# Kernel optimization log

Hardware: AMD Instinct MI355X
Metric: run time of the kernel (lower is better)

The kernel has to match this reference:

```python
import jax, jax.numpy as jnp
import numpy as np

D_MODEL = 512
NHEAD = 8
HEAD_DIM = D_MODEL // NHEAD  # 64
BUCKETS = 32                 # lsh_hash_bucket_size; hashes >= 32 never attended (faithful to source loop)
N_HASHES = 2
B, T = 2, 2048


def setup_inputs() -> dict:
    key = jax.random.key(0)
    ks = jax.random.split(key, 14)
    s = 1.0 / np.sqrt(D_MODEL)
    sh = 1.0 / np.sqrt(HEAD_DIM)
    return {
        "query": jax.random.normal(ks[0], (B, T, D_MODEL), dtype=jnp.float32),
        "key": jax.random.normal(ks[1], (B, T, D_MODEL), dtype=jnp.float32),
        "value": jax.random.normal(ks[2], (B, T, D_MODEL), dtype=jnp.float32),
        "Wq": jax.random.normal(ks[3], (D_MODEL, D_MODEL), dtype=jnp.float32) * s,
        "bq": jnp.zeros((D_MODEL,), jnp.float32),
        "Wk": jax.random.normal(ks[4], (D_MODEL, D_MODEL), dtype=jnp.float32) * s,
        "bk": jnp.zeros((D_MODEL,), jnp.float32),
        "Wv": jax.random.normal(ks[5], (D_MODEL, D_MODEL), dtype=jnp.float32) * s,
        "bv": jnp.zeros((D_MODEL,), jnp.float32),
        "Wo": jax.random.normal(ks[6], (D_MODEL, D_MODEL), dtype=jnp.float32) * s,
        "bo": jnp.zeros((D_MODEL,), jnp.float32),
        "lsh_W": jax.random.normal(ks[7], (N_HASHES, HEAD_DIM, HEAD_DIM), dtype=jnp.float32) * sh,
        "lsh_b": jax.random.normal(ks[8], (N_HASHES, HEAD_DIM), dtype=jnp.float32) * sh,
    }


def reference(query, key, value, Wq, bq, Wk, bk, Wv, bv, Wo, bo, lsh_W, lsh_b):
    B0, Nt, E = query.shape
    H, Dh = NHEAD, E // NHEAD

    def lin(x, W, b):  # torch nn.Linear: x @ W.T + b
        return x @ W.T + b

    # Source transposes (0,1) then reshape(B0, Nt, H, Dh); reshape on the
    # contiguous transposed tensor == jnp reshape of swapaxes result.
    q = lin(jnp.swapaxes(query, 0, 1), Wq, bq).reshape(B0, Nt, H, Dh).transpose(0, 2, 1, 3)
    k = lin(jnp.swapaxes(key, 0, 1), Wk, bk).reshape(B0, Nt, H, Dh).transpose(0, 2, 1, 3)
    v = lin(jnp.swapaxes(value, 0, 1), Wv, bv).reshape(B0, Nt, H, Dh).transpose(0, 2, 1, 3)

    scale = 1.0 / jnp.sqrt(jnp.asarray(Dh, q.dtype))
    neg = jnp.finfo(q.dtype).min
    acc = jnp.zeros_like(q)
    for i in range(N_HASHES):
        # argmax(softmax(x)) == argmax(x)
        qh = jnp.argmax(q @ lsh_W[i].T + lsh_b[i], axis=-1)  # [B,H,T]
        kh = jnp.argmax(k @ lsh_W[i].T + lsh_b[i], axis=-1)  # [B,H,T]
        # attend only within same bucket AND bucket id < BUCKETS (source loops 0..BUCKETS-1)
        mask = (qh[..., :, None] == kh[..., None, :]) & (qh[..., :, None] < BUCKETS)
        scores = jnp.einsum('bhtd,bhsd->bhts', q, k) * scale
        probs = jax.nn.softmax(jnp.where(mask, scores, neg), axis=-1)
        valid = mask.any(axis=-1)  # queries with >=1 key in-bucket; others stay zero
        out_i = jnp.einsum('bhts,bhsd->bhtd', probs, v)
        acc = acc + jnp.where(valid[..., None], out_i, jnp.zeros((), q.dtype))
    out = acc / N_HASHES  # mean over hash rounds

    out = out.transpose(0, 2, 1, 3).reshape(B0, Nt, E)
    out = lin(out, Wo, bo)
    return jnp.swapaxes(out, 0, 1)  # [Nt, B0, E]
```

## Files before the change

kernel.cpp:

```cpp
#include <hip/hip_runtime.h>
#include <stdint.h>
#include <math.h>


#define T_ 2048
#define E_ 512
#define H_ 8
#define DH_ 64
#define B_ 2
#define M_ 4096
#define NROUND 2
#define NBUCKET 32
#define NSEG 32
#define MAXTASK 5120

typedef short v8s __attribute__((ext_vector_type(8)));
typedef _Float16 v8h __attribute__((ext_vector_type(8)));
typedef float v4f __attribute__((ext_vector_type(4)));

__device__ __forceinline__ float bf2f(uint16_t u) {
  union { uint32_t i; float f; } v; v.i = ((uint32_t)u) << 16; return v.f;
}
__device__ __forceinline__ uint16_t f2bf(float f) {
  union { float fv; uint32_t i; } v; v.fv = f;
  uint32_t x = v.i;
  x += 0x7fffu + ((x >> 16) & 1u);
  return (uint16_t)(x >> 16);
}
__device__ __forceinline__ void split8(const float4 a, const float4 b,
                                       v8s& h, v8s& l) {
  const float x[8] = {a.x, a.y, a.z, a.w, b.x, b.y, b.z, b.w};
#pragma unroll
  for (int j = 0; j < 8; j++) {
    const uint16_t hh = f2bf(x[j]);
    h[j] = (short)hh;
    l[j] = (short)f2bf(x[j] - bf2f(hh));
  }
}
__device__ __forceinline__ void split2h8(const float4 a, const float4 b,
                                         v8h& h, v8h& l) {
  const float x[8] = {a.x, a.y, a.z, a.w, b.x, b.y, b.z, b.w};
#pragma unroll
  for (int j = 0; j < 8; j++) {
    const float xv = x[j];
    const _Float16 hh = (fabsf(xv) < 6.1035156e-5f) ? (_Float16)0.0f
                                                    : (_Float16)xv;
    const float r = xv - (float)hh;
    h[j] = hh;
    l[j] = (_Float16)(r * 4096.0f);
  }
}

__global__ __launch_bounds__(256) void prep_kernel(
    const float* __restrict__ Xq, const float* __restrict__ Xk,
    const float* __restrict__ Xv,
    const float* __restrict__ Wq, const float* __restrict__ Wk,
    const float* __restrict__ Wv, const float* __restrict__ Wo,
    const float* __restrict__ lshW,
    uint16_t* __restrict__ Xqh, uint16_t* __restrict__ Xql,
    uint16_t* __restrict__ Xkh, uint16_t* __restrict__ Xkl,
    uint16_t* __restrict__ Xvh, uint16_t* __restrict__ Xvl,
    uint16_t* __restrict__ Wqh, uint16_t* __restrict__ Wql,
    uint16_t* __restrict__ Wkh, uint16_t* __restrict__ Wkl,
    uint16_t* __restrict__ Wvh, uint16_t* __restrict__ Wvl,
    uint16_t* __restrict__ Woh, uint16_t* __restrict__ Wol,
    uint16_t* __restrict__ Lwh, uint16_t* __restrict__ Lwl,
    float* __restrict__ attn, int* __restrict__ cnt)
{
  const int bid = blockIdx.x;
  const int tid = threadIdx.x;

  if (bid < 3072) {
    const int sel = bid >> 10;
    const float* X = (sel == 0) ? Xq : (sel == 1) ? Xk : Xv;
    uint16_t* H = (sel == 0) ? Xqh : (sel == 1) ? Xkh : Xvh;
    uint16_t* L = (sel == 0) ? Xql : (sel == 1) ? Xkl : Xvl;
    const int e = ((bid & 1023) * 256 + tid) * 8;
    const int p = e >> 9, k = e & 511;
    const long src = ((long)(p & 1) * T_ + (p >> 1)) * E_ + k;
    const float4 a = *(const float4*)(X + src);
    const float4 b = *(const float4*)(X + src + 4);
    v8h h, l;
    split2h8(a, b, h, l);
    const long to = ((long)((p >> 5) * 32 + (k >> 5) * 2 + ((p >> 4) & 1)) * 64
                     + ((k >> 3) & 3) * 16 + (p & 15)) * 8;
    *(v8h*)(H + to) = h;
    *(v8h*)(L + to) = l;
    return;
  }

  if (bid < 3584) {
    const int wsel = (bid - 3072) >> 7;
    const int e = (((bid - 3072) & 127) * 256 + tid) * 8;
    const int n = e >> 9, k = e & 511;
    const long to = ((long)((n >> 4) * 16 + (k >> 5)) * 64
                     + ((k >> 3) & 3) * 16 + (n & 15)) * 8;
    if (wsel < 3) {
      const float* S = (wsel == 0) ? Wq : (wsel == 1) ? Wk : Wv;
      const float4 a = *(const float4*)(S + e);
      const float4 b = *(const float4*)(S + e + 4);
      v8h h, l;
      split2h8(a, b, h, l);
      uint16_t* H = (wsel == 0) ? Wqh : (wsel == 1) ? Wkh : Wvh;
      uint16_t* L = (wsel == 0) ? Wql : (wsel == 1) ? Wkl : Wvl;
      *(v8h*)(H + to) = h;
      *(v8h*)(L + to) = l;
    } else {
      const float4 a = *(const float4*)(Wo + e);
      const float4 b = *(const float4*)(Wo + e + 4);
      v8s h, l;
      split8(a, b, h, l);
      *(v8s*)(Woh + to) = h;
      *(v8s*)(Wol + to) = l;
    }
    return;
  }

  if (bid < 4608) {
    float4* a4 = (float4*)attn;
    const int g = (bid - 3584) * 512 + tid * 2;
    a4[g] = make_float4(0.f, 0.f, 0.f, 0.f);
    a4[g + 1] = make_float4(0.f, 0.f, 0.f, 0.f);
    return;
  }

  for (int i = tid; i < 2 * NSEG * NBUCKET + 1; i += 256) cnt[i] = 0;
  for (int i = tid; i < NROUND * DH_ * DH_; i += 256) {
    const float xv = lshW[i];
    const _Float16 hh = (fabsf(xv) < 6.1035156e-5f) ? (_Float16)0.0f
                                                    : (_Float16)xv;
    const float r = xv - (float)hh;
    *(_Float16*)(Lwh + i) = hh;
    *(_Float16*)(Lwl + i) = (_Float16)(r * 4096.0f);
  }
}

__global__ __launch_bounds__(256) void proj_mfma(
    const uint16_t* __restrict__ Aqh, const uint16_t* __restrict__ Aql,
    const uint16_t* __restrict__ Akh, const uint16_t* __restrict__ Akl,
    const uint16_t* __restrict__ Avh, const uint16_t* __restrict__ Avl,
    const uint16_t* __restrict__ Bqh, const uint16_t* __restrict__ Bql,
    const uint16_t* __restrict__ Bkh, const uint16_t* __restrict__ Bkl,
    const uint16_t* __restrict__ Bvh, const uint16_t* __restrict__ Bvl,
    const float* __restrict__ bq, const float* __restrict__ bk,
    const float* __restrict__ bv,
    float* __restrict__ Qo, float* __restrict__ Ko, float* __restrict__ Vo)
{
  const uint16_t *Ah, *Al, *Bh, *Bl;
  const float* bias; float* C;
  if (blockIdx.z == 0)      { Ah = Aqh; Al = Aql; Bh = Bqh; Bl = Bql; bias = bq; C = Qo; }
  else if (blockIdx.z == 1) { Ah = Akh; Al = Akl; Bh = Bkh; Bl = Bkl; bias = bk; C = Ko; }
  else                      { Ah = Avh; Al = Avl; Bh = Bvh; Bl = Bvl; bias = bv; C = Vo; }

  const int wid = threadIdx.x >> 6, lane = threadIdx.x & 63;
  const int mb = blockIdx.x * 4 + wid;
  const int nb0 = blockIdx.y * 4;
  const int m0 = mb * 32, n0 = blockIdx.y * 64;
  const int l15 = lane & 15, quad = lane >> 4;

  const long aB = (long)mb * 16384 + lane * 8;
  long bB[4];
#pragma unroll
  for (int j = 0; j < 4; j++) bB[j] = (long)(nb0 + j) * 8192 + lane * 8;

  v4f accH[2][4] = {};
  v4f accX[2][4] = {};

  v8h ah0 = *(const v8h*)(Ah + aB);
  v8h ah1 = *(const v8h*)(Ah + aB + 512);
  v8h al0 = *(const v8h*)(Al + aB);
  v8h al1 = *(const v8h*)(Al + aB + 512);
  v8h bh[4], bl[4];
#pragma unroll
  for (int j = 0; j < 4; j++) {
    bh[j] = *(const v8h*)(Bh + bB[j]);
    bl[j] = *(const v8h*)(Bl + bB[j]);
  }

  for (int ks = 0; ks < 16; ks++) {
    const int kn = (ks + 1) & 15;
    const v8h nah0 = *(const v8h*)(Ah + aB + kn * 1024);
    const v8h nah1 = *(const v8h*)(Ah + aB + kn * 1024 + 512);
    const v8h nal0 = *(const v8h*)(Al + aB + kn * 1024);
    const v8h nal1 = *(const v8h*)(Al + aB + kn * 1024 + 512);
    v8h nbh[4], nbl[4];
#pragma unroll
    for (int j = 0; j < 4; j++) {
      nbh[j] = *(const v8h*)(Bh + bB[j] + kn * 512);
      nbl[j] = *(const v8h*)(Bl + bB[j] + kn * 512);
    }

#pragma unroll
    for (int j = 0; j < 4; j++) {
      accH[0][j] = __builtin_amdgcn_mfma_f32_16x16x32_f16(ah0, bh[j], accH[0][j], 0, 0, 0);
      accH[1][j] = __builtin_amdgcn_mfma_f32_16x16x32_f16(ah1, bh[j], accH[1][j], 0, 0, 0);
    }
#pragma unroll
    for (int j = 0; j < 4; j++) {
      accX[0][j] = __builtin_amdgcn_mfma_f32_16x16x32_f16(ah0, bl[j], accX[0][j], 0, 0, 0);
      accX[1][j] = __builtin_amdgcn_mfma_f32_16x16x32_f16(ah1, bl[j], accX[1][j], 0, 0, 0);
    }
#pragma unroll
    for (int j = 0; j < 4; j++) {
      accX[0][j] = __builtin_amdgcn_mfma_f32_16x16x32_f16(al0, bh[j], accX[0][j], 0, 0, 0);
      accX[1][j] = __builtin_amdgcn_mfma_f32_16x16x32_f16(al1, bh[j], accX[1][j], 0, 0, 0);
    }

    ah0 = nah0; al0 = nal0; ah1 = nah1; al1 = nal1;
#pragma unroll
    for (int j = 0; j < 4; j++) { bh[j] = nbh[j]; bl[j] = nbl[j]; }
  }

#pragma unroll
  for (int i = 0; i < 2; i++)
#pragma unroll
    for (int j = 0; j < 4; j++) {
      const int colg = n0 + j * 16 + l15;
      const float bb = bias[colg];
#pragma unroll
      for (int r = 0; r < 4; r++) {
        const int mm = m0 + i * 16 + quad * 4 + r;
        C[(long)mm * E_ + colg] =
            accH[i][j][r] + accX[i][j][r] * (1.0f / 4096.0f) + bb;
      }
    }
}

__global__ __launch_bounds__(256) void mfma_gemm(
    const float* __restrict__ A,
    const uint16_t* __restrict__ Bht, const uint16_t* __restrict__ Blt,
    const float* __restrict__ bias, float* __restrict__ C)
{
  const int wid = threadIdx.x >> 6, lane = threadIdx.x & 63;
  const int m0 = (blockIdx.x * 4 + wid) * 32;
  const int nb0 = blockIdx.y * 4;
  const int n0 = blockIdx.y * 64;
  const int l15 = lane & 15, quad = lane >> 4;

  const long sa0 = (long)(m0 + l15) * E_ + quad * 8;
  const long sa1 = sa0 + 16L * E_;
  long bB[4];
#pragma unroll
  for (int j = 0; j < 4; j++) bB[j] = (long)(nb0 + j) * 8192 + lane * 8;

  v4f acc[2][4] = {};
  for (int ks = 0; ks < 16; ks++) {
    const int k0 = ks * 32;
    v8s ah0, al0, ah1, al1;
    split8(*(const float4*)(A + sa0 + k0), *(const float4*)(A + sa0 + k0 + 4),
           ah0, al0);
    split8(*(const float4*)(A + sa1 + k0), *(const float4*)(A + sa1 + k0 + 4),
           ah1, al1);
    v8s bh[4], bl[4];
#pragma unroll
    for (int j = 0; j < 4; j++) {
      bh[j] = *(const v8s*)(Bht + bB[j] + ks * 512);
      bl[j] = *(const v8s*)(Blt + bB[j] + ks * 512);
    }
#pragma unroll
    for (int j = 0; j < 4; j++) {
      acc[0][j] = __builtin_amdgcn_mfma_f32_16x16x32_bf16(ah0, bh[j], acc[0][j], 0, 0, 0);
      acc[1][j] = __builtin_amdgcn_mfma_f32_16x16x32_bf16(ah1, bh[j], acc[1][j], 0, 0, 0);
    }
#pragma unroll
    for (int j = 0; j < 4; j++) {
      acc[0][j] = __builtin_amdgcn_mfma_f32_16x16x32_bf16(ah0, bl[j], acc[0][j], 0, 0, 0);
      acc[1][j] = __builtin_amdgcn_mfma_f32_16x16x32_bf16(ah1, bl[j], acc[1][j], 0, 0, 0);
    }
#pragma unroll
    for (int j = 0; j < 4; j++) {
      acc[0][j] = __builtin_amdgcn_mfma_f32_16x16x32_bf16(al0, bh[j], acc[0][j], 0, 0, 0);
      acc[1][j] = __builtin_amdgcn_mfma_f32_16x16x32_bf16(al1, bh[j], acc[1][j], 0, 0, 0);
    }
  }

#pragma unroll
  for (int i = 0; i < 2; i++)
#pragma unroll
    for (int j = 0; j < 4; j++) {
      const int colg = n0 + j * 16 + l15;
      const float bb = bias[colg];
#pragma unroll
      for (int r = 0; r < 4; r++) {
        const int mm = m0 + i * 16 + quad * 4 + r;
        const int crow = (mm & (T_ - 1)) * B_ + (mm >> 11);
        C[(long)crow * E_ + colg] = acc[i][j][r] + bb;
      }
    }
}

__global__ __launch_bounds__(256) void hash_mfma(
    const float* __restrict__ Q, const float* __restrict__ K,
    const uint16_t* __restrict__ Lwh, const uint16_t* __restrict__ Lwl,
    const float* __restrict__ lshb,
    int* __restrict__ qh, int* __restrict__ kh,
    int* __restrict__ qcnt, int* __restrict__ kcnt)
{
  const int comb = blockIdx.y;
  const int src = comb >> 1, r = comb & 1;
  const float* X = src ? K : Q;
  int* outh = src ? kh : qh;
  int* cnt  = src ? kcnt : qcnt;

  const int wid = threadIdx.x >> 6, lane = threadIdx.x & 63;
  const int m0 = (blockIdx.x * 4 + wid) * 32;
  const int l15 = lane & 15, quad = lane >> 4;

  v8h bh[4][2], bl[4][2];
#pragma unroll
  for (int n = 0; n < 4; n++)
#pragma unroll
    for (int k = 0; k < 2; k++) {
      const int o = r * (DH_ * DH_) + (n * 16 + l15) * DH_ + k * 32 + quad * 8;
      bh[n][k] = *(const v8h*)(Lwh + o);
      bl[n][k] = *(const v8h*)(Lwl + o);
    }

  v4f accH[2][4] = {};
  v4f accX[2][4] = {};
#pragma unroll
  for (int k = 0; k < 2; k++) {
    const long a0 = (long)(m0 + l15) * DH_ + k * 32 + quad * 8;
    const long a1 = a0 + 16L * DH_;
    v8h ah0, al0, ah1, al1;
    split2h8(*(const float4*)(X + a0), *(const float4*)(X + a0 + 4), ah0, al0);
    split2h8(*(const float4*)(X + a1), *(const float4*)(X + a1 + 4), ah1, al1);
#pragma unroll
    for (int n = 0; n < 4; n++) {
      accH[0][n] = __builtin_amdgcn_mfma_f32_16x16x32_f16(ah0, bh[n][k], accH[0][n], 0, 0, 0);
      accH[1][n] = __builtin_amdgcn_mfma_f32_16x16x32_f16(ah1, bh[n][k], accH[1][n], 0, 0, 0);
      accX[0][n] = __builtin_amdgcn_mfma_f32_16x16x32_f16(ah0, bl[n][k], accX[0][n], 0, 0, 0);
      accX[1][n] = __builtin_amdgcn_mfma_f32_16x16x32_f16(ah1, bl[n][k], accX[1][n], 0, 0, 0);
      accX[0][n] = __builtin_amdgcn_mfma_f32_16x16x32_f16(al0, bh[n][k], accX[0][n], 0, 0, 0);
      accX[1][n] = __builtin_amdgcn_mfma_f32_16x16x32_f16(al1, bh[n][k], accX[1][n], 0, 0, 0);
    }
  }

  float bb[4];
#pragma unroll
  for (int n = 0; n < 4; n++) bb[n] = lshb[r * DH_ + n * 16 + l15];

#pragma unroll
  for (int i = 0; i < 2; i++)
#pragma unroll
    for (int reg = 0; reg < 4; reg++) {
      float bv = -INFINITY; int bi = 0x7fffffff;
#pragma unroll
      for (int n = 0; n < 4; n++) {
        const float v = accH[i][n][reg] + accX[i][n][reg] * (1.0f / 4096.0f)
                        + bb[n];
        const int idx = n * 16 + l15;
        if (v > bv || (v == bv && idx < bi)) { bv = v; bi = idx; }
      }
#pragma unroll
      for (int d = 8; d >= 1; d >>= 1) {
        const float ov = __shfl_xor(bv, d);
        const int oi = __shfl_xor(bi, d);
        if (ov > bv || (ov == bv && oi < bi)) { bv = ov; bi = oi; }
      }
      if (l15 == 0) {
        const int hr = m0 + i * 16 + quad * 4 + reg;
        const int p = hr >> 3, hh = hr & 7;
        const int bt = p >> 11, t = p & (T_ - 1);
        const int seg = r * 16 + bt * H_ + hh;
        outh[seg * T_ + t] = bi;
        if (bi < NBUCKET) atomicAdd(&cnt[seg * NBUCKET + bi], 1);
      }
    }
}

__global__ __launch_bounds__(1024) void scan_kernel(
    const int* __restrict__ kcnt, int* __restrict__ koff,
    int* __restrict__ kcur,
    const int* __restrict__ qcnt, int* __restrict__ qoff,
    int* __restrict__ qcur,
    int* __restrict__ ntasks, int* __restrict__ tasks)
{
  const int tid = threadIdx.x;
  const int isq = blockIdx.x;
  const int seg = tid >> 5;
  const int b   = tid & 31;
  const int* cnt = isq ? qcnt : kcnt;
  int* off = isq ? qoff : koff;
  int* cur = isq ? qcur : kcur;

  const int c = cnt[seg * NBUCKET + b];

  int s = c;
#pragma unroll
  for (int d = 1; d < 32; d <<= 1) {
    const int t = __shfl_up(s, d, 32);
    if (b >= d) s += t;
  }
  const int excl = s - c;
  off[seg * (NBUCKET + 1) + b] = excl;
  cur[seg * NBUCKET + b] = excl;
  if (b == 31) off[seg * (NBUCKET + 1) + NBUCKET] = s;

  if (isq) {
    const int nt = (c + 15) >> 4;
    const int lane = tid & 63;
    int ws = nt;
#pragma unroll
    for (int d = 1; d < 64; d <<= 1) {
      const int t = __shfl_up(ws, d, 64);
      if (lane >= d) ws += t;
    }
    const int wtotal = __shfl(ws, 63, 64);
    int base = 0;
    if (lane == 63 && wtotal > 0) base = atomicAdd(ntasks, wtotal);
    base = __shfl(base, 63, 64);
    const int my = base + ws - nt;
    for (int i = 0; i < nt; i++)
      tasks[my + i] = (seg << 16) | (b << 8) | i;
  }
}

__global__ __launch_bounds__(256) void scatter2_kernel(
    const int* __restrict__ kh, const int* __restrict__ qh,
    int* __restrict__ kcur, int* __restrict__ qcur,
    int* __restrict__ klist, int* __restrict__ qlist)
{
  const int idx = blockIdx.x * 256 + threadIdx.x;
  const int y = blockIdx.y;
  const int* hsh = y ? qh : kh;
  int* cur = y ? qcur : kcur;
  int* list = y ? qlist : klist;
  const int v = hsh[idx];
  if (v < NBUCKET) {
    const int seg = idx >> 11;
    const int pos = atomicAdd(&cur[seg * NBUCKET + v], 1);
    list[seg * T_ + pos] = idx & (T_ - 1);
  }
}

__global__ __launch_bounds__(256) void attn_task(
    const float* __restrict__ Q, const float* __restrict__ K,
    const float* __restrict__ V,
    const int* __restrict__ qlist, const int* __restrict__ qoff,
    const int* __restrict__ klist, const int* __restrict__ koff,
    const int* __restrict__ tasks, const int* __restrict__ ntasks,
    float* __restrict__ attn)
{
  __shared__ __align__(16) float QPs[16 * 68];
  __shared__ __align__(16) float Ks[64 * 68];
  __shared__ __align__(16) float Vs[64 * 68];

  if ((int)blockIdx.x >= *ntasks) return;
  const int tk = tasks[blockIdx.x];
  const int seg = tk >> 16, bucket = (tk >> 8) & 255, qt = tk & 255;
  const int ctx = seg & 15;
  const int b = ctx >> 3, h = ctx & 7;

  const int qlo = qoff[seg * (NBUCKET + 1) + bucket] + qt * 16;
  const int nqt = min(16, qoff[seg * (NBUCKET + 1) + bucket + 1] - qlo);
  const int klo = koff[seg * (NBUCKET + 1) + bucket];
  const int nk  = koff[seg * (NBUCKET + 1) + bucket + 1] - klo;
  if (nk == 0) return;

  const int tid = threadIdx.x;
  const int qrow = tid >> 4, col = tid & 15;
  const float* Qb = Q + ((long)b * T_) * E_ + h * DH_;
  const float* Kb = K + ((long)b * T_) * E_ + h * DH_;
  const float* Vb = V + ((long)b * T_) * E_ + h * DH_;
  const int* ql = qlist + seg * T_;
  const int* kl = klist + seg * T_;

  {
    float4 v = make_float4(0.f, 0.f, 0.f, 0.f);
    if (qrow < nqt) v = *(const float4*)(Qb + (long)ql[qlo + qrow] * E_ + col * 4);
    *(float4*)&QPs[qrow * 68 + col * 4] = v;
  }
  __syncthreads();
  float4 qreg[16];
#pragma unroll
  for (int i = 0; i < 16; i++) qreg[i] = *(const float4*)&QPs[qrow * 68 + i * 4];

  float l = 0.f;
  float4 o = make_float4(0.f, 0.f, 0.f, 0.f);

  for (int kt = 0; kt < nk; kt += 64) {
    const int nkt = min(64, nk - kt);
    __syncthreads();
#pragma unroll
    for (int it = 0; it < 4; it++) {
      const int fidx = it * 256 + tid;
      const int row = fidx >> 4, c4 = fidx & 15;
      if (row < nkt) {
        const long src = (long)kl[klo + kt + row] * E_ + c4 * 4;
        *(float4*)&Ks[row * 68 + c4 * 4] = *(const float4*)(Kb + src);
        *(float4*)&Vs[row * 68 + c4 * 4] = *(const float4*)(Vb + src);
      } else {
        *(float4*)&Vs[row * 68 + c4 * 4] = make_float4(0.f, 0.f, 0.f, 0.f);
      }
    }
    __syncthreads();
#pragma unroll
    for (int kk = 0; kk < 4; kk++) {
      const int k = kk * 16 + col;
      float p = 0.f;
      if (k < nkt) {
        const float* kp = &Ks[k * 68];
        float s = 0.f;
#pragma unroll
        for (int d4 = 0; d4 < 16; d4++) {
          const float4 c = *(const float4*)(kp + d4 * 4);
          s += qreg[d4].x * c.x + qreg[d4].y * c.y +
               qreg[d4].z * c.z + qreg[d4].w * c.w;
        }
        p = __expf(s * 0.125f);
      }
      QPs[qrow * 68 + k] = p;
    }
    __syncthreads();
    const int nk4 = (nkt + 3) >> 2;
#pragma unroll 2
    for (int k4 = 0; k4 < nk4; k4++) {
      const float4 pk = *(const float4*)&QPs[qrow * 68 + k4 * 4];
      const float4 v0 = *(const float4*)&Vs[(k4 * 4 + 0) * 68 + col * 4];
      const float4 v1 = *(const float4*)&Vs[(k4 * 4 + 1) * 68 + col * 4];
      const float4 v2 = *(const float4*)&Vs[(k4 * 4 + 2) * 68 + col * 4];
      const float4 v3 = *(const float4*)&Vs[(k4 * 4 + 3) * 68 + col * 4];
      l += (pk.x + pk.y) + (pk.z + pk.w);
      o.x += pk.x * v0.x + pk.y * v1.x + pk.z * v2.x + pk.w * v3.x;
      o.y += pk.x * v0.y + pk.y * v1.y + pk.z * v2.y + pk.w * v3.y;
      o.z += pk.x * v0.z + pk.y * v1.z + pk.z * v2.z + pk.w * v3.z;
      o.w += pk.x * v0.w + pk.y * v1.w + pk.z * v2.w + pk.w * v3.w;
    }
  }

  if (qrow < nqt) {
    const float inv = 0.5f / l;
    const int t = ql[qlo + qrow];
    float* op = attn + ((long)b * T_ + t) * E_ + h * DH_ + col * 4;
    atomicAdd(op + 0, o.x * inv);
    atomicAdd(op + 1, o.y * inv);
    atomicAdd(op + 2, o.z * inv);
    atomicAdd(op + 3, o.w * inv);
  }
}

extern "C" void kernel_launch(void* const* d_in, const int* in_sizes, int n_in,
                              void* d_out, int out_size, void* d_ws, size_t ws_size,
                              hipStream_t stream) {
  const float* query = (const float*)d_in[0];
  const float* key   = (const float*)d_in[1];
  const float* value = (const float*)d_in[2];
  const float* Wq = (const float*)d_in[3];
  const float* bq = (const float*)d_in[4];
  const float* Wk = (const float*)d_in[5];
  const float* bk = (const float*)d_in[6];
  const float* Wv = (const float*)d_in[7];
  const float* bv = (const float*)d_in[8];
  const float* Wo = (const float*)d_in[9];
  const float* bo = (const float*)d_in[10];
  const float* lshW = (const float*)d_in[11];
  const float* lshb = (const float*)d_in[12];

  const size_t MSZ = (size_t)M_ * E_;
  const size_t WSZ = (size_t)E_ * E_;
  float* Q    = (float*)d_ws;
  float* K    = Q + MSZ;
  float* V    = K + MSZ;
  float* attn = V + MSZ;
  int* qh     = (int*)(attn + MSZ);
  int* kh     = qh + NSEG * T_;
  int* klist  = kh + NSEG * T_;
  int* qlist  = klist + NSEG * T_;
  int* kcnt   = qlist + NSEG * T_;
  int* qcnt   = kcnt + NSEG * NBUCKET;
  int* ntasks = qcnt + NSEG * NBUCKET;
  int* kcur   = ntasks + 1;
  int* qcur   = kcur + NSEG * NBUCKET;
  int* koff   = qcur + NSEG * NBUCKET;
  int* qoff   = koff + NSEG * (NBUCKET + 1);
  int* tasks  = qoff + NSEG * (NBUCKET + 1);
  uint16_t* Woh = (uint16_t*)(((uintptr_t)(tasks + MAXTASK) + 15) & ~(uintptr_t)15);
  uint16_t* Wol = Woh + WSZ;
  uint16_t* Wqh = Wol + WSZ;
  uint16_t* Wql = Wqh + WSZ;
  uint16_t* Wkh = Wql + WSZ;
  uint16_t* Wkl = Wkh + WSZ;
  uint16_t* Wvh = Wkl + WSZ;
  uint16_t* Wvl = Wvh + WSZ;
  uint16_t* Xqh = Wvl + WSZ;
  uint16_t* Xql = Xqh + MSZ;
  uint16_t* Xkh = Xql + MSZ;
  uint16_t* Xkl = Xkh + MSZ;
  uint16_t* Xvh = Xkl + MSZ;
  uint16_t* Xvl = Xvh + MSZ;
  uint16_t* Lwh = Xvl + MSZ;
  uint16_t* Lwl = Lwh + (size_t)NROUND * DH_ * DH_;

  prep_kernel<<<dim3(4609), 256, 0, stream>>>(
      query, key, value, Wq, Wk, Wv, Wo, lshW,
      Xqh, Xql, Xkh, Xkl, Xvh, Xvl,
      Wqh, Wql, Wkh, Wkl, Wvh, Wvl, Woh, Wol,
      Lwh, Lwl, attn, kcnt);
  proj_mfma<<<dim3(M_ / 128, E_ / 64, 3), 256, 0, stream>>>(
      Xqh, Xql, Xkh, Xkl, Xvh, Xvl,
      Wqh, Wql, Wkh, Wkl, Wvh, Wvl,
      bq, bk, bv, Q, K, V);
  hash_mfma<<<dim3(M_ * H_ / 128, 4), 256, 0, stream>>>(
      Q, K, Lwh, Lwl, lshb, qh, kh, qcnt, kcnt);
  scan_kernel<<<dim3(2), 1024, 0, stream>>>(kcnt, koff, kcur, qcnt, qoff, qcur,
                                            ntasks, tasks);
  scatter2_kernel<<<dim3(NSEG * T_ / 256, 2), 256, 0, stream>>>(
      kh, qh, kcur, qcur, klist, qlist);
  attn_task<<<dim3(MAXTASK), 256, 0, stream>>>(
      Q, K, V, qlist, qoff, klist, koff, tasks, ntasks, attn);
  mfma_gemm<<<dim3(M_ / 128, E_ / 64), 256, 0, stream>>>(
      attn, Woh, Wol, bo, (float*)d_out);
}
```

Baseline: 239.9 us.

## Compute bucketed attention tile with split-bf16 MFMA instead of scalar FP32

```diff
diff --git a/kernel.cpp b/kernel.cpp
--- a/kernel.cpp
+++ b/kernel.cpp
@@ -442,9 +442,9 @@
     const int* __restrict__ tasks, const int* __restrict__ ntasks,
     float* __restrict__ attn)
 {
-  __shared__ __align__(16) float QPs[16 * 68];
-  __shared__ __align__(16) float Ks[64 * 68];
-  __shared__ __align__(16) float Vs[64 * 68];
+  __shared__ __align__(16) float Plds[16][68];
+  __shared__ __align__(16) float Vts[64][68];
+  __shared__ float larr[16];
 
   if ((int)blockIdx.x >= *ntasks) return;
   const int tk = tasks[blockIdx.x];
@@ -459,84 +459,114 @@
   if (nk == 0) return;
 
   const int tid = threadIdx.x;
-  const int qrow = tid >> 4, col = tid & 15;
+  const int wid = tid >> 6, lane = tid & 63;
+  const int l15 = lane & 15, quad = lane >> 4;
+  const int r0 = tid >> 4, c4 = tid & 15;
+
   const float* Qb = Q + ((long)b * T_) * E_ + h * DH_;
   const float* Kb = K + ((long)b * T_) * E_ + h * DH_;
   const float* Vb = V + ((long)b * T_) * E_ + h * DH_;
   const int* ql = qlist + seg * T_;
   const int* kl = klist + seg * T_;
 
-  {
-    float4 v = make_float4(0.f, 0.f, 0.f, 0.f);
-    if (qrow < nqt) v = *(const float4*)(Qb + (long)ql[qlo + qrow] * E_ + col * 4);
-    *(float4*)&QPs[qrow * 68 + col * 4] = v;
+  if (tid < 16) larr[tid] = 0.f;
+
+  const long qrow = (long)ql[qlo + min(l15, nqt - 1)] * E_;
+  v8s qfh[2], qfl[2];
+#pragma unroll
+  for (int ks = 0; ks < 2; ks++) {
+    const float4 a = *(const float4*)(Qb + qrow + ks * 32 + quad * 8);
+    const float4 c = *(const float4*)(Qb + qrow + ks * 32 + quad * 8 + 4);
+    split8(a, c, qfh[ks], qfl[ks]);
   }
   __syncthreads();
-  float4 qreg[16];
-#pragma unroll
-  for (int i = 0; i < 16; i++) qreg[i] = *(const float4*)&QPs[qrow * 68 + i * 4];
-
-  float l = 0.f;
-  float4 o = make_float4(0.f, 0.f, 0.f, 0.f);
+
+  v4f oacc = {0.f, 0.f, 0.f, 0.f};
 
   for (int kt = 0; kt < nk; kt += 64) {
-    const int nkt = min(64, nk - kt);
+    float4 vreg[4];
+#pragma unroll
+    for (int it = 0; it < 4; it++) {
+      const int key = kt + it * 16 + r0;
+      const long krow = (long)kl[klo + min(key, nk - 1)] * E_;
+      vreg[it] = *(const float4*)(Vb + krow + c4 * 4);
+    }
+
+    const int keyg = kt + wid * 16 + l15;
+    const long krow = (long)kl[klo + min(keyg, nk - 1)] * E_;
+    v4f sacc = {0.f, 0.f, 0.f, 0.f};
+#pragma unroll
+    for (int ks = 0; ks < 2; ks++) {
+      const float4 a = *(const float4*)(Kb + krow + ks * 32 + quad * 8);
+      const float4 c = *(const float4*)(Kb + krow + ks * 32 + quad * 8 + 4);
+      v8s kfh, kfl;
+      split8(a, c, kfh, kfl);
+      sacc = __builtin_amdgcn_mfma_f32_16x16x32_bf16(qfh[ks], kfh, sacc, 0, 0, 0);
+      sacc = __builtin_amdgcn_mfma_f32_16x16x32_bf16(qfh[ks], kfl, sacc, 0, 0, 0);
+      sacc = __builtin_amdgcn_mfma_f32_16x16x32_bf16(qfl[ks], kfh, sacc, 0, 0, 0);
+    }
+
+    const bool kvalid = keyg < nk;
+    const float p0 = kvalid ? __expf(sacc[0] * 0.125f) : 0.f;
+    const float p1 = kvalid ? __expf(sacc[1] * 0.125f) : 0.f;
+    const float p2 = kvalid ? __expf(sacc[2] * 0.125f) : 0.f;
+    const float p3 = kvalid ? __expf(sacc[3] * 0.125f) : 0.f;
+
+    float rs0 = p0, rs1 = p1, rs2 = p2, rs3 = p3;
+#pragma unroll
+    for (int d = 1; d < 16; d <<= 1) {
+      rs0 += __shfl_xor(rs0, d);
+      rs1 += __shfl_xor(rs1, d);
+      rs2 += __shfl_xor(rs2, d);
+      rs3 += __shfl_xor(rs3, d);
+    }
+    if (l15 == 0) {
+      atomicAdd(&larr[quad * 4 + 0], rs0);
+      atomicAdd(&larr[quad * 4 + 1], rs1);
+      atomicAdd(&larr[quad * 4 + 2], rs2);
+      atomicAdd(&larr[quad * 4 + 3], rs3);
+    }
+    Plds[quad * 4 + 0][wid * 16 + l15] = p0;
+    Plds[quad * 4 + 1][wid * 16 + l15] = p1;
+    Plds[quad * 4 + 2][wid * 16 + l15] = p2;
+    Plds[quad * 4 + 3][wid * 16 + l15] = p3;
+
+#pragma unroll
+    for (int it = 0; it < 4; it++) {
+      const int row = it * 16 + r0;
+      Vts[c4 * 4 + 0][row] = vreg[it].x;
+      Vts[c4 * 4 + 1][row] = vreg[it].y;
+      Vts[c4 * 4 + 2][row] = vreg[it].z;
+      Vts[c4 * 4 + 3][row] = vreg[it].w;
+    }
     __syncthreads();
-#pragma unroll
-    for (int it = 0; it < 4; it++) {
-      const int fidx = it * 256 + tid;
-      const int row = fidx >> 4, c4 = fidx & 15;
-      if (row < nkt) {
-        const long src = (long)kl[klo + kt + row] * E_ + c4 * 4;
-        *(float4*)&Ks[row * 68 + c4 * 4] = *(const float4*)(Kb + src);
-        *(float4*)&Vs[row * 68 + c4 * 4] = *(const float4*)(Vb + src);
-      } else {
-        *(float4*)&Vs[row * 68 + c4 * 4] = make_float4(0.f, 0.f, 0.f, 0.f);
-      }
+
+#pragma unroll
+    for (int ks = 0; ks < 2; ks++) {
+      const float4 pa = *(const float4*)&Plds[l15][ks * 32 + quad * 8];
+      const float4 pb = *(const float4*)&Plds[l15][ks * 32 + quad * 8 + 4];
+      v8s pah, pal;
+      split8(pa, pb, pah, pal);
+      const float4 va = *(const float4*)&Vts[wid * 16 + l15][ks * 32 + quad * 8];
+      const float4 vb = *(const float4*)&Vts[wid * 16 + l15][ks * 32 + quad * 8 + 4];
+      v8s vfh, vfl;
+      split8(va, vb, vfh, vfl);
+      oacc = __builtin_amdgcn_mfma_f32_16x16x32_bf16(pah, vfh, oacc, 0, 0, 0);
+      oacc = __builtin_amdgcn_mfma_f32_16x16x32_bf16(pah, vfl, oacc, 0, 0, 0);
+      oacc = __builtin_amdgcn_mfma_f32_16x16x32_bf16(pal, vfh, oacc, 0, 0, 0);
     }
     __syncthreads();
-#pragma unroll
-    for (int kk = 0; kk < 4; kk++) {
-      const int k = kk * 16 + col;
-      float p = 0.f;
-      if (k < nkt) {
-        const float* kp = &Ks[k * 68];
-        float s = 0.f;
-#pragma unroll
-        for (int d4 = 0; d4 < 16; d4++) {
-          const float4 c = *(const float4*)(kp + d4 * 4);
-          s += qreg[d4].x * c.x + qreg[d4].y * c.y +
-               qreg[d4].z * c.z + qreg[d4].w * c.w;
-        }
-        p = __expf(s * 0.125f);
-      }
-      QPs[qrow * 68 + k] = p;
-    }
-    __syncthreads();
-    const int nk4 = (nkt + 3) >> 2;
-#pragma unroll 2
-    for (int k4 = 0; k4 < nk4; k4++) {
-      const float4 pk = *(const float4*)&QPs[qrow * 68 + k4 * 4];
-      const float4 v0 = *(const float4*)&Vs[(k4 * 4 + 0) * 68 + col * 4];
-      const float4 v1 = *(const float4*)&Vs[(k4 * 4 + 1) * 68 + col * 4];
-      const float4 v2 = *(const float4*)&Vs[(k4 * 4 + 2) * 68 + col * 4];
-      const float4 v3 = *(const float4*)&Vs[(k4 * 4 + 3) * 68 + col * 4];
-      l += (pk.x + pk.y) + (pk.z + pk.w);
-      o.x += pk.x * v0.x + pk.y * v1.x + pk.z * v2.x + pk.w * v3.x;
-      o.y += pk.x * v0.y + pk.y * v1.y + pk.z * v2.y + pk.w * v3.y;
-      o.z += pk.x * v0.z + pk.y * v1.z + pk.z * v2.z + pk.w * v3.z;
-      o.w += pk.x * v0.w + pk.y * v1.w + pk.z * v2.w + pk.w * v3.w;
-    }
-  }
-
-  if (qrow < nqt) {
-    const float inv = 0.5f / l;
-    const int t = ql[qlo + qrow];
-    float* op = attn + ((long)b * T_ + t) * E_ + h * DH_ + col * 4;
-    atomicAdd(op + 0, o.x * inv);
-    atomicAdd(op + 1, o.y * inv);
-    atomicAdd(op + 2, o.z * inv);
-    atomicAdd(op + 3, o.w * inv);
+  }
+
+#pragma unroll
+  for (int r = 0; r < 4; r++) {
+    const int q = quad * 4 + r;
+    if (q < nqt) {
+      const float inv = 0.5f / larr[q];
+      const int t = ql[qlo + q];
+      atomicAdd(attn + ((long)b * T_ + t) * E_ + h * DH_ + wid * 16 + l15,
+                oacc[r] * inv);
+    }
   }
 }
 
```

Measured after the change: 223.9 us. 6.7% less time.
